# Kernel optimization log

Hardware: AMD Instinct MI355X
Metric: run time of the kernel (lower is better)

Reference implementation:

```python
import jax, jax.numpy as jnp
import numpy as np

N_CUST = 500000
N_FUND = 50000
N_EDGE = 4000000
D_CUST = 101
D_FUND = 1
HID = 64


def setup_inputs() -> dict:
    key = jax.random.key(0)
    ks = jax.random.split(key, 16)
    s = lambda fan_in: 1.0 / np.sqrt(fan_in)
    return {
        "x_customer": jax.random.normal(ks[0], (N_CUST, D_CUST), jnp.float32),
        "x_fund": jax.random.normal(ks[1], (N_FUND, D_FUND), jnp.float32),
        "src_fund": jax.random.randint(ks[2], (N_EDGE,), 0, N_FUND, jnp.int64),
        "dst_customer": jax.random.randint(ks[3], (N_EDGE,), 0, N_CUST, jnp.int64),
        # per-node-type input projections
        "W_cust": jax.random.uniform(ks[4], (D_CUST, HID), jnp.float32, -s(D_CUST), s(D_CUST)),
        "b_cust": jax.random.uniform(ks[5], (HID,), jnp.float32, -s(D_CUST), s(D_CUST)),
        "W_fund": jax.random.uniform(ks[6], (D_FUND, HID), jnp.float32, -s(D_FUND), s(D_FUND)),
        "b_fund": jax.random.uniform(ks[7], (HID,), jnp.float32, -s(D_FUND), s(D_FUND)),
        # SAGEConv fund->customer: lin_l (neighbor aggr, bias) + lin_r (self, no bias)
        "W_l": jax.random.uniform(ks[8], (HID, HID), jnp.float32, -s(HID), s(HID)),
        "b_l": jax.random.uniform(ks[9], (HID,), jnp.float32, -s(HID), s(HID)),
        "W_r": jax.random.uniform(ks[10], (HID, HID), jnp.float32, -s(HID), s(HID)),
        # output head
        "W_out": jax.random.uniform(ks[11], (HID, 2), jnp.float32, -s(HID), s(HID)),
        "b_out": jax.random.uniform(ks[12], (2,), jnp.float32, -s(HID), s(HID)),
    }


def reference(x_customer, x_fund, src_fund, dst_customer,
              W_cust, b_cust, W_fund, b_fund, W_l, b_l, W_r, W_out, b_out):
    # per-node-type linear + relu
    h_c = jax.nn.relu(x_customer @ W_cust + b_cust)  # [N_CUST, HID]
    h_f = jax.nn.relu(x_fund @ W_fund + b_fund)      # [N_FUND, HID]

    # SAGEConv (fund -> customer): gather src fund features per edge,
    # mean-aggregate by destination customer (scatter-sum / count)
    msgs = h_f[src_fund]  # [N_EDGE, HID]
    summed = jax.ops.segment_sum(msgs, dst_customer, num_segments=N_CUST)
    cnt = jax.ops.segment_sum(jnp.ones((msgs.shape[0],), msgs.dtype),
                              dst_customer, num_segments=N_CUST)
    mean = summed / jnp.maximum(cnt, 1.0)[:, None]

    out_c = mean @ W_l + b_l + h_c @ W_r  # SAGE: lin_l(aggr) + lin_r(self)
    return out_c @ W_out + b_out          # [N_CUST, 2]
```

## Files before the change

kernel.cpp:

```cpp
#include <hip/hip_runtime.h>
#include <stdint.h>

#define N_CUST 500000
#define N_FUND 50000
#define N_EDGE 4000000
#define D_CUST 101
#define HID 64

#define NB   512
#define EPB  ((N_EDGE + NB - 1) / NB)
#define CB   512
#define NBKT ((N_CUST + CB - 1) / CB)
#define CAP  5120
#define GPAD 32

typedef float float4u __attribute__((ext_vector_type(4), aligned(4)));
using frag_ab = __attribute__((ext_vector_type(8))) short;
using frag_cd = __attribute__((ext_vector_type(4))) float;

struct __align__(16) Accum { float g0, g1, cnt, pad; };

__device__ __forceinline__ short f2bf(float f) {
    unsigned u = __float_as_uint(f);
    u += 0x7fffu + ((u >> 16) & 1u);
    return (short)(u >> 16);
}

__global__ __launch_bounds__(256) void k_gf(
    const float* __restrict__ x_fund,
    const float* __restrict__ W_fund,
    const float* __restrict__ b_fund,
    const float* __restrict__ W_l,
    const float* __restrict__ W_r,
    const float* __restrict__ W_out,
    const float* __restrict__ Wc,
    const float* __restrict__ b_l,
    const float* __restrict__ b_out,
    float2* __restrict__ gf,
    frag_ab* __restrict__ wcb,
    float* __restrict__ Bt,
    float* __restrict__ c2,
    unsigned* __restrict__ gcur,
    float4* __restrict__ Az)
{
    __shared__ float sAf[128];
    __shared__ float sWf[64];
    __shared__ float sBf[64];
    int t = threadIdx.x;

    if (Az != nullptr) {
        float4 z4 = make_float4(0.f, 0.f, 0.f, 0.f);
        for (int i = blockIdx.x * 256 + t; i < N_CUST; i += gridDim.x * 256)
            Az[i] = z4;
    }

    if (t < 128) {
        int h = t >> 1, j = t & 1;
        float s = 0.f;
        for (int k = 0; k < 64; ++k)
            s = fmaf(W_l[h * 64 + k], W_out[k * 2 + j], s);
        sAf[t] = s;
    } else if (t < 192) {
        sWf[t - 128] = W_fund[t - 128];
    } else {
        sBf[t - 192] = b_fund[t - 192];
    }
    __syncthreads();

    int f = blockIdx.x * 256 + t;
    if (f < N_FUND) {
        float xf = x_fund[f];
        float g0 = 0.f, g1 = 0.f;
        #pragma unroll
        for (int h = 0; h < 64; ++h) {
            float hf = fmaxf(fmaf(xf, sWf[h], sBf[h]), 0.f);
            g0 = fmaf(hf, sAf[2 * h + 0], g0);
            g1 = fmaf(hf, sAf[2 * h + 1], g1);
        }
        gf[f] = make_float2(g0, g1);
    }

    if (blockIdx.x == 0) {
        for (int k = t; k < NBKT * GPAD; k += 256) gcur[k] = 0u;
        if (t < 128) {
            int h = t >> 1, j = t & 1;
            float s = 0.f;
            for (int k = 0; k < 64; ++k)
                s = fmaf(W_r[h * 64 + k], W_out[k * 2 + j], s);
            Bt[t] = s;
        } else if (t < 130) {
            int j = t - 128;
            float s = b_out[j];
            for (int k = 0; k < 64; ++k)
                s = fmaf(b_l[k], W_out[k * 2 + j], s);
            c2[j] = s;
        }
        for (int sidx = t; sidx < 1024; sidx += 256) {
            int fidx = sidx >> 6, l = sidx & 63;
            int c = l & 15, q = l >> 4;
            int nt = fidx >> 2, kc = fidx & 3;
            frag_ab fr;
            #pragma unroll
            for (int j = 0; j < 8; ++j) {
                int kk = kc * 32 + q * 8 + j;
                int h  = nt * 16 + c;
                fr[j] = (kk < D_CUST) ? f2bf(Wc[kk * HID + h]) : (short)0;
            }
            wcb[sidx] = fr;
        }
    }
}

__global__ __launch_bounds__(256) void k_reorder(
    const int* __restrict__ src, const int* __restrict__ dst,
    unsigned* __restrict__ gcur, unsigned* __restrict__ recs)
{
    __shared__ unsigned hist[NBKT];
    __shared__ unsigned localOff[NBKT];
    __shared__ unsigned cur[NBKT];
    __shared__ unsigned baseG[NBKT];
    __shared__ unsigned ldsRec[EPB];
    __shared__ unsigned short ldsBkt[EPB];

    int t = threadIdx.x, b = blockIdx.x;
    int e0 = b * EPB, e1 = min(e0 + EPB, N_EDGE);
    int cntE = e1 - e0;

    for (int k = t; k < NBKT; k += 256) hist[k] = 0;
    __syncthreads();
    for (int e = e0 + t; e < e1; e += 256)
        atomicAdd(&hist[((unsigned)dst[e]) >> 9], 1u);
    __syncthreads();

    if (t < 64) {
        unsigned v[16], pre[16], run = 0;
        #pragma unroll
        for (int j = 0; j < 16; ++j) {
            int idx = t * 16 + j;
            v[j] = (idx < NBKT) ? hist[idx] : 0u;
            pre[j] = run; run += v[j];
        }
        unsigned sc = run;
        #pragma unroll
        for (int d = 1; d < 64; d <<= 1) {
            unsigned n = __shfl_up(sc, d, 64);
            if (t >= d) sc += n;
        }
        unsigned lane_excl = sc - run;
        #pragma unroll
        for (int j = 0; j < 16; ++j) {
            int idx = t * 16 + j;
            if (idx < NBKT) {
                localOff[idx] = lane_excl + pre[j];
                cur[idx]      = lane_excl + pre[j];
            }
        }
    }
    __syncthreads();

    for (int k = t; k < NBKT; k += 256) {
        unsigned h = hist[k];
        baseG[k] = h ? ((unsigned)k * CAP + atomicAdd(&gcur[k * GPAD], h)) : 0u;
    }

    for (int e = e0 + t; e < e1; e += 256) {
        unsigned d = (unsigned)dst[e];
        unsigned s = (unsigned)src[e];
        unsigned k = d >> 9;
        unsigned p = atomicAdd(&cur[k], 1u);
        ldsRec[p] = s | ((d & 511u) << 16);
        ldsBkt[p] = (unsigned short)k;
    }
    __syncthreads();

    for (int i = t; i < cntE; i += 256) {
        unsigned k = ldsBkt[i];
        unsigned g = baseG[k] + (i - localOff[k]);
        if (g < (k + 1u) * CAP) recs[g] = ldsRec[i];
    }
}

__global__ __launch_bounds__(256) void k_bucket(
    const unsigned* __restrict__ recs, const unsigned* __restrict__ gcur,
    const float2* __restrict__ gf,
    const float* __restrict__ x, const float* __restrict__ bc,
    const frag_ab* __restrict__ wcb, const float* __restrict__ Bt,
    const float* __restrict__ c2,
    float2* __restrict__ out)
{
    __shared__ float s0[CB], s1[CB], scn[CB];
    __shared__ float sBt[128];
    __shared__ float pbuf[2 * CB];
    __shared__ float zb[3][16 * 68];

    int t = threadIdx.x, k = blockIdx.x;
    int w = t >> 6, lane = t & 63;
    int c = lane & 15, q = lane >> 4;

    if (t < 128) sBt[t] = Bt[t];
    for (int cc = t; cc < CB; cc += 256) { s0[cc] = 0.f; s1[cc] = 0.f; scn[cc] = 0.f; }
    __syncthreads();

    int cust0 = k * CB;
    int ncust = min(CB, N_CUST - cust0);
    int n_tiles = ncust >> 4;

    if (w == 3) {
        unsigned n = min(gcur[(unsigned)k * GPAD], (unsigned)CAP);
        const unsigned* rp = recs + (size_t)k * CAP;
        unsigned i = (unsigned)lane * 4u;
        for (; i + 4u <= n; i += 256u) {
            uint4 rr = *(const uint4*)(rp + i);
            float2 ga = gf[rr.x & 0xFFFFu];
            float2 gb = gf[rr.y & 0xFFFFu];
            float2 gc = gf[rr.z & 0xFFFFu];
            float2 gd = gf[rr.w & 0xFFFFu];
            unsigned da = rr.x >> 16, db = rr.y >> 16;
            unsigned dc = rr.z >> 16, dd = rr.w >> 16;
            atomicAdd(&s0[da], ga.x); atomicAdd(&s1[da], ga.y); atomicAdd(&scn[da], 1.f);
            atomicAdd(&s0[db], gb.x); atomicAdd(&s1[db], gb.y); atomicAdd(&scn[db], 1.f);
            atomicAdd(&s0[dc], gc.x); atomicAdd(&s1[dc], gc.y); atomicAdd(&scn[dc], 1.f);
            atomicAdd(&s0[dd], gd.x); atomicAdd(&s1[dd], gd.y); atomicAdd(&scn[dd], 1.f);
        }
        unsigned base = n & ~3u;
        if ((unsigned)lane < (n & 3u)) {
            unsigned r = rp[base + lane];
            float2 g = gf[r & 0xFFFFu];
            unsigned dl = r >> 16;
            atomicAdd(&s0[dl], g.x); atomicAdd(&s1[dl], g.y); atomicAdd(&scn[dl], 1.f);
        }
    } else {
        float* z = zb[w];
        frag_ab bfrag[16];
        #pragma unroll
        for (int f = 0; f < 16; ++f) bfrag[f] = wcb[f * 64 + lane];
        float bcv[4];
        #pragma unroll
        for (int nt = 0; nt < 4; ++nt) bcv[nt] = bc[nt * 16 + c];
        float c20 = c2[0], c21 = c2[1];

        for (int tl = w; tl < n_tiles; tl += 3) {
            int lrow = tl * 16 + c;
            int row = cust0 + lrow;
            const float* xr = x + (size_t)row * D_CUST;
            frag_ab af[4];
            #pragma unroll
            for (int kc = 0; kc < 3; ++kc) {
                float4u lo = *(const float4u*)(xr + kc * 32 + q * 8);
                float4u hi = *(const float4u*)(xr + kc * 32 + q * 8 + 4);
                frag_ab f;
                f[0]=f2bf(lo[0]); f[1]=f2bf(lo[1]); f[2]=f2bf(lo[2]); f[3]=f2bf(lo[3]);
                f[4]=f2bf(hi[0]); f[5]=f2bf(hi[1]); f[6]=f2bf(hi[2]); f[7]=f2bf(hi[3]);
                af[kc] = f;
            }
            {
                frag_ab f = {0,0,0,0,0,0,0,0};
                if (q == 0) {
                    float4u lo = *(const float4u*)(xr + 96);
                    f[0]=f2bf(lo[0]); f[1]=f2bf(lo[1]); f[2]=f2bf(lo[2]); f[3]=f2bf(lo[3]);
                    f[4]=f2bf(xr[100]);
                }
                af[3] = f;
            }
            frag_cd acc[4];
            #pragma unroll
            for (int nt = 0; nt < 4; ++nt)
                acc[nt] = (frag_cd){bcv[nt], bcv[nt], bcv[nt], bcv[nt]};
            #pragma unroll
            for (int kc = 0; kc < 4; ++kc)
                #pragma unroll
                for (int nt = 0; nt < 4; ++nt)
                    acc[nt] = __builtin_amdgcn_mfma_f32_16x16x32_bf16(
                        af[kc], bfrag[nt * 4 + kc], acc[nt], 0, 0, 0);

            #pragma unroll
            for (int nt = 0; nt < 4; ++nt)
                #pragma unroll
                for (int i = 0; i < 4; ++i)
                    z[(q * 4 + i) * 68 + nt * 16 + c] = fmaxf(acc[nt][i], 0.f);

            float p0 = 0.f, p1 = 0.f;
            #pragma unroll
            for (int j4 = 0; j4 < 4; ++j4) {
                float4u zv = *(const float4u*)(z + c * 68 + q * 16 + j4 * 4);
                float4u b0 = *(const float4u*)(sBt + q * 32 + j4 * 8);
                float4u b1 = *(const float4u*)(sBt + q * 32 + j4 * 8 + 4);
                p0 = fmaf(zv[0], b0[0], p0); p1 = fmaf(zv[0], b0[1], p1);
                p0 = fmaf(zv[1], b0[2], p0); p1 = fmaf(zv[1], b0[3], p1);
                p0 = fmaf(zv[2], b1[0], p0); p1 = fmaf(zv[2], b1[1], p1);
                p0 = fmaf(zv[3], b1[2], p0); p1 = fmaf(zv[3], b1[3], p1);
            }
            p0 += __shfl_xor(p0, 16, 64); p0 += __shfl_xor(p0, 32, 64);
            p1 += __shfl_xor(p1, 16, 64); p1 += __shfl_xor(p1, 32, 64);
            if (q == 0) {
                pbuf[2 * lrow]     = p0 + c20;
                pbuf[2 * lrow + 1] = p1 + c21;
            }
        }
    }
    __syncthreads();

    for (int cc = t; cc < ncust; cc += 256) {
        float inv = 1.0f / fmaxf(scn[cc], 1.0f);
        out[cust0 + cc] = make_float2(fmaf(s0[cc], inv, pbuf[2 * cc]),
                                      fmaf(s1[cc], inv, pbuf[2 * cc + 1]));
    }
}

__global__ __launch_bounds__(256) void k_scatter_direct(
    const int* __restrict__ src, const int* __restrict__ dst,
    const float2* __restrict__ gf, Accum* __restrict__ A)
{
    int stride = gridDim.x * 256;
    for (int e = blockIdx.x * 256 + threadIdx.x; e < N_EDGE; e += stride) {
        int s = src[e], d = dst[e];
        float2 g = gf[s];
        unsafeAtomicAdd(&A[d].g0, g.x);
        unsafeAtomicAdd(&A[d].g1, g.y);
        unsafeAtomicAdd(&A[d].cnt, 1.0f);
    }
}

__global__ __launch_bounds__(256) void k_mean(
    const Accum* __restrict__ A, float2* __restrict__ mean2)
{
    int i = blockIdx.x * 256 + threadIdx.x;
    if (i < N_CUST) {
        Accum a = A[i];
        float inv = 1.0f / fmaxf(a.cnt, 1.0f);
        mean2[i] = make_float2(a.g0 * inv, a.g1 * inv);
    }
}

__global__ __launch_bounds__(256) void k_gemm(
    const float* __restrict__ x, const float* __restrict__ bc,
    const frag_ab* __restrict__ wcb, const float* __restrict__ Bt,
    const float* __restrict__ c2, const float2* __restrict__ mean2,
    float2* __restrict__ out)
{
    __shared__ float sBt[128];
    __shared__ float zb[4][16 * 68];

    int t = threadIdx.x;
    int w = t >> 6, lane = t & 63;
    int c = lane & 15, q = lane >> 4;
    float* z = zb[w];

    if (t < 128) sBt[t] = Bt[t];
    frag_ab bfrag[16];
    #pragma unroll
    for (int f = 0; f < 16; ++f) bfrag[f] = wcb[f * 64 + lane];
    float bcv[4];
    #pragma unroll
    for (int nt = 0; nt < 4; ++nt) bcv[nt] = bc[nt * 16 + c];
    float c20 = c2[0], c21 = c2[1];
    __syncthreads();

    const int NT = N_CUST / 16;
    for (int tl = blockIdx.x * 4 + w; tl < NT; tl += gridDim.x * 4) {
        int row0 = tl * 16;
        const float* xr = x + (size_t)(row0 + c) * D_CUST;
        frag_ab af[4];
        #pragma unroll
        for (int kc = 0; kc < 3; ++kc) {
            float4u lo = *(const float4u*)(xr + kc * 32 + q * 8);
            float4u hi = *(const float4u*)(xr + kc * 32 + q * 8 + 4);
            frag_ab f;
            f[0]=f2bf(lo[0]); f[1]=f2bf(lo[1]); f[2]=f2bf(lo[2]); f[3]=f2bf(lo[3]);
            f[4]=f2bf(hi[0]); f[5]=f2bf(hi[1]); f[6]=f2bf(hi[2]); f[7]=f2bf(hi[3]);
            af[kc] = f;
        }
        {
            frag_ab f = {0,0,0,0,0,0,0,0};
            if (q == 0) {
                float4u lo = *(const float4u*)(xr + 96);
                f[0]=f2bf(lo[0]); f[1]=f2bf(lo[1]); f[2]=f2bf(lo[2]); f[3]=f2bf(lo[3]);
                f[4]=f2bf(xr[100]);
            }
            af[3] = f;
        }
        frag_cd acc[4];
        #pragma unroll
        for (int nt = 0; nt < 4; ++nt)
            acc[nt] = (frag_cd){bcv[nt], bcv[nt], bcv[nt], bcv[nt]};
        #pragma unroll
        for (int kc = 0; kc < 4; ++kc)
            #pragma unroll
            for (int nt = 0; nt < 4; ++nt)
                acc[nt] = __builtin_amdgcn_mfma_f32_16x16x32_bf16(
                    af[kc], bfrag[nt * 4 + kc], acc[nt], 0, 0, 0);
        #pragma unroll
        for (int nt = 0; nt < 4; ++nt)
            #pragma unroll
            for (int i = 0; i < 4; ++i)
                z[(q * 4 + i) * 68 + nt * 16 + c] = fmaxf(acc[nt][i], 0.f);
        float p0 = 0.f, p1 = 0.f;
        #pragma unroll
        for (int j4 = 0; j4 < 4; ++j4) {
            float4u zv = *(const float4u*)(z + c * 68 + q * 16 + j4 * 4);
            float4u b0 = *(const float4u*)(sBt + q * 32 + j4 * 8);
            float4u b1 = *(const float4u*)(sBt + q * 32 + j4 * 8 + 4);
            p0 = fmaf(zv[0], b0[0], p0); p1 = fmaf(zv[0], b0[1], p1);
            p0 = fmaf(zv[1], b0[2], p0); p1 = fmaf(zv[1], b0[3], p1);
            p0 = fmaf(zv[2], b1[0], p0); p1 = fmaf(zv[2], b1[1], p1);
            p0 = fmaf(zv[3], b1[2], p0); p1 = fmaf(zv[3], b1[3], p1);
        }
        p0 += __shfl_xor(p0, 16, 64); p0 += __shfl_xor(p0, 32, 64);
        p1 += __shfl_xor(p1, 16, 64); p1 += __shfl_xor(p1, 32, 64);
        if (q == 0) {
            float2 m = mean2[row0 + c];
            out[row0 + c] = make_float2(p0 + c20 + m.x, p1 + c21 + m.y);
        }
    }
}

extern "C" void kernel_launch(void* const* d_in, const int* in_sizes, int n_in,
                              void* d_out, int out_size, void* d_ws, size_t ws_size,
                              hipStream_t stream) {
    const float* x_customer = (const float*)d_in[0];
    const float* x_fund     = (const float*)d_in[1];
    const int*   src_fund   = (const int*)d_in[2];
    const int*   dst_cust   = (const int*)d_in[3];
    const float* W_cust     = (const float*)d_in[4];
    const float* b_cust     = (const float*)d_in[5];
    const float* W_fund     = (const float*)d_in[6];
    const float* b_fund     = (const float*)d_in[7];
    const float* W_l        = (const float*)d_in[8];
    const float* b_l        = (const float*)d_in[9];
    const float* W_r        = (const float*)d_in[10];
    const float* W_out      = (const float*)d_in[11];
    const float* b_out      = (const float*)d_in[12];

    char* ws = (char*)d_ws;
    const size_t NEED_FAST = 20550976ull;

    if (ws_size >= NEED_FAST) {
        unsigned* recs = (unsigned*)(ws);
        float2*   gf   = (float2*)  (ws + 20008960);
        frag_ab*  wcb  = (frag_ab*) (ws + 20408960);
        float*    Bt   = (float*)   (ws + 20425344);
        float*    c2   = (float*)   (ws + 20425856);
        unsigned* gcur = (unsigned*)(ws + 20425920);

        k_gf<<<256, 256, 0, stream>>>(
            x_fund, W_fund, b_fund, W_l, W_r, W_out, W_cust, b_l, b_out,
            gf, wcb, Bt, c2, gcur, nullptr);
        k_reorder<<<NB, 256, 0, stream>>>(src_fund, dst_cust, gcur, recs);
        k_bucket<<<NBKT, 256, 0, stream>>>(
            recs, gcur, gf, x_customer, b_cust, wcb, Bt, c2, (float2*)d_out);
    } else {
        Accum*    A    = (Accum*)   (ws);
        float2*   mn2  = (float2*)  (ws + 8000000);
        float2*   gf   = (float2*)  (ws + 12000000);
        frag_ab*  wcb  = (frag_ab*) (ws + 12400000);
        float*    Bt   = (float*)   (ws + 12416384);
        float*    c2   = (float*)   (ws + 12416896);
        unsigned* gcur = (unsigned*)(ws + 12416960);

        k_gf<<<256, 256, 0, stream>>>(
            x_fund, W_fund, b_fund, W_l, W_r, W_out, W_cust, b_l, b_out,
            gf, wcb, Bt, c2, gcur, (float4*)A);
        k_scatter_direct<<<2048, 256, 0, stream>>>(src_fund, dst_cust, gf, A);
        k_mean<<<(N_CUST + 255) / 256, 256, 0, stream>>>(A, mn2);
        k_gemm<<<2048, 256, 0, stream>>>(
            x_customer, b_cust, wcb, Bt, c2, mn2, (float2*)d_out);
    }
}
```

Before: 420.3 us.

## Share MFMA tile work across all waves via LDS counter, reduce epilogue in registers

Waves now claim 16-row projection tiles from a shared LDS counter, so the scatter wave also picks up GEMM tiles once its edge loop finishes, rather than three waves owning fixed tiles. The ReLU and output-head dot product are now computed straight from the MFMA accumulators with 16-lane shuffle reductions, removing the LDS staging buffer and the shared Bt copy. Launch bounds request 6 blocks per CU to raise occupancy. In exchange the scatter wave now holds the weight fragments, there are more shuffles per tile, and register pressure is tighter under the occupancy hint.

Result: slower. 485.4 us (+15.5%).

```diff
diff --git a/kernel.cpp b/kernel.cpp
--- a/kernel.cpp
+++ b/kernel.cpp
@@ -180,7 +180,7 @@
     }
 }
 
-__global__ __launch_bounds__(256) void k_bucket(
+__global__ __launch_bounds__(256, 6) void k_bucket(
     const unsigned* __restrict__ recs, const unsigned* __restrict__ gcur,
     const float2* __restrict__ gf,
     const float* __restrict__ x, const float* __restrict__ bc,
@@ -189,17 +189,30 @@
     float2* __restrict__ out)
 {
     __shared__ float s0[CB], s1[CB], scn[CB];
-    __shared__ float sBt[128];
     __shared__ float pbuf[2 * CB];
-    __shared__ float zb[3][16 * 68];
+    __shared__ int tileCtr;
 
     int t = threadIdx.x, k = blockIdx.x;
     int w = t >> 6, lane = t & 63;
     int c = lane & 15, q = lane >> 4;
 
-    if (t < 128) sBt[t] = Bt[t];
+    if (t == 0) tileCtr = 0;
     for (int cc = t; cc < CB; cc += 256) { s0[cc] = 0.f; s1[cc] = 0.f; scn[cc] = 0.f; }
     __syncthreads();
+
+    frag_ab bfrag[16];
+    #pragma unroll
+    for (int f = 0; f < 16; ++f) bfrag[f] = wcb[f * 64 + lane];
+    float btv[8];
+    #pragma unroll
+    for (int nt = 0; nt < 4; ++nt) {
+        btv[2 * nt]     = Bt[(nt * 16 + c) * 2];
+        btv[2 * nt + 1] = Bt[(nt * 16 + c) * 2 + 1];
+    }
+    float bcv[4];
+    #pragma unroll
+    for (int nt = 0; nt < 4; ++nt) bcv[nt] = bc[nt * 16 + c];
+    float c20 = c2[0], c21 = c2[1];
 
     int cust0 = k * CB;
     int ncust = min(CB, N_CUST - cust0);
@@ -229,70 +242,62 @@
             unsigned dl = r >> 16;
             atomicAdd(&s0[dl], g.x); atomicAdd(&s1[dl], g.y); atomicAdd(&scn[dl], 1.f);
         }
-    } else {
-        float* z = zb[w];
-        frag_ab bfrag[16];
-        #pragma unroll
-        for (int f = 0; f < 16; ++f) bfrag[f] = wcb[f * 64 + lane];
-        float bcv[4];
-        #pragma unroll
-        for (int nt = 0; nt < 4; ++nt) bcv[nt] = bc[nt * 16 + c];
-        float c20 = c2[0], c21 = c2[1];
-
-        for (int tl = w; tl < n_tiles; tl += 3) {
-            int lrow = tl * 16 + c;
-            int row = cust0 + lrow;
-            const float* xr = x + (size_t)row * D_CUST;
-            frag_ab af[4];
-            #pragma unroll
-            for (int kc = 0; kc < 3; ++kc) {
-                float4u lo = *(const float4u*)(xr + kc * 32 + q * 8);
-                float4u hi = *(const float4u*)(xr + kc * 32 + q * 8 + 4);
-                frag_ab f;
+    }
+
+    for (;;) {
+        int tl;
+        if (lane == 0) tl = atomicAdd(&tileCtr, 1);
+        tl = __shfl(tl, 0, 64);
+        if (tl >= n_tiles) break;
+
+        int row = cust0 + tl * 16 + c;
+        const float* xr = x + (size_t)row * D_CUST;
+        frag_ab af[4];
+        #pragma unroll
+        for (int kc = 0; kc < 3; ++kc) {
+            float4u lo = *(const float4u*)(xr + kc * 32 + q * 8);
+            float4u hi = *(const float4u*)(xr + kc * 32 + q * 8 + 4);
+            frag_ab f;
+            f[0]=f2bf(lo[0]); f[1]=f2bf(lo[1]); f[2]=f2bf(lo[2]); f[3]=f2bf(lo[3]);
+            f[4]=f2bf(hi[0]); f[5]=f2bf(hi[1]); f[6]=f2bf(hi[2]); f[7]=f2bf(hi[3]);
+            af[kc] = f;
+        }
+        {
+            frag_ab f = {0,0,0,0,0,0,0,0};
+            if (q == 0) {
+                float4u lo = *(const float4u*)(xr + 96);
                 f[0]=f2bf(lo[0]); f[1]=f2bf(lo[1]); f[2]=f2bf(lo[2]); f[3]=f2bf(lo[3]);
-                f[4]=f2bf(hi[0]); f[5]=f2bf(hi[1]); f[6]=f2bf(hi[2]); f[7]=f2bf(hi[3]);
-                af[kc] = f;
-            }
-            {
-                frag_ab f = {0,0,0,0,0,0,0,0};
-                if (q == 0) {
-                    float4u lo = *(const float4u*)(xr + 96);
-                    f[0]=f2bf(lo[0]); f[1]=f2bf(lo[1]); f[2]=f2bf(lo[2]); f[3]=f2bf(lo[3]);
-                    f[4]=f2bf(xr[100]);
-                }
-                af[3] = f;
-            }
-            frag_cd acc[4];
+                f[4]=f2bf(xr[100]);
+            }
+            af[3] = f;
+        }
+        frag_cd acc[4];
+        #pragma unroll
+        for (int nt = 0; nt < 4; ++nt)
+            acc[nt] = (frag_cd){bcv[nt], bcv[nt], bcv[nt], bcv[nt]};
+        #pragma unroll
+        for (int kc = 0; kc < 4; ++kc)
             #pragma unroll
             for (int nt = 0; nt < 4; ++nt)
-                acc[nt] = (frag_cd){bcv[nt], bcv[nt], bcv[nt], bcv[nt]};
-            #pragma unroll
-            for (int kc = 0; kc < 4; ++kc)
-                #pragma unroll
-                for (int nt = 0; nt < 4; ++nt)
-                    acc[nt] = __builtin_amdgcn_mfma_f32_16x16x32_bf16(
-                        af[kc], bfrag[nt * 4 + kc], acc[nt], 0, 0, 0);
-
-            #pragma unroll
-            for (int nt = 0; nt < 4; ++nt)
-                #pragma unroll
-                for (int i = 0; i < 4; ++i)
-                    z[(q * 4 + i) * 68 + nt * 16 + c] = fmaxf(acc[nt][i], 0.f);
-
+                acc[nt] = __builtin_amdgcn_mfma_f32_16x16x32_bf16(
+                    af[kc], bfrag[nt * 4 + kc], acc[nt], 0, 0, 0);
+
+        #pragma unroll
+        for (int i = 0; i < 4; ++i) {
             float p0 = 0.f, p1 = 0.f;
             #pragma unroll
-            for (int j4 = 0; j4 < 4; ++j4) {
-                float4u zv = *(const float4u*)(z + c * 68 + q * 16 + j4 * 4);
-                float4u b0 = *(const float4u*)(sBt + q * 32 + j4 * 8);
-                float4u b1 = *(const float4u*)(sBt + q * 32 + j4 * 8 + 4);
-                p0 = fmaf(zv[0], b0[0], p0); p1 = fmaf(zv[0], b0[1], p1);
-                p0 = fmaf(zv[1], b0[2], p0); p1 = fmaf(zv[1], b0[3], p1);
-                p0 = fmaf(zv[2], b1[0], p0); p1 = fmaf(zv[2], b1[1], p1);
-                p0 = fmaf(zv[3], b1[2], p0); p1 = fmaf(zv[3], b1[3], p1);
-            }
-            p0 += __shfl_xor(p0, 16, 64); p0 += __shfl_xor(p0, 32, 64);
-            p1 += __shfl_xor(p1, 16, 64); p1 += __shfl_xor(p1, 32, 64);
-            if (q == 0) {
+            for (int nt = 0; nt < 4; ++nt) {
+                float zv = fmaxf(acc[nt][i], 0.f);
+                p0 = fmaf(zv, btv[2 * nt],     p0);
+                p1 = fmaf(zv, btv[2 * nt + 1], p1);
+            }
+            #pragma unroll
+            for (int m = 1; m < 16; m <<= 1) {
+                p0 += __shfl_xor(p0, m, 16);
+                p1 += __shfl_xor(p1, m, 16);
+            }
+            if (c == 0) {
+                int lrow = tl * 16 + q * 4 + i;
                 pbuf[2 * lrow]     = p0 + c20;
                 pbuf[2 * lrow + 1] = p1 + c21;
             }
```
